# Kernel optimization log

Measured on AMD Instinct MI355X. Metric: run time of the kernel, lower is better.

The kernel has to match this reference:

```python
import jax, jax.numpy as jnp
import numpy as np
import math

B, S, H, N = 64, 512, 768, 16
C_COMP, C_REL = 5, 3
P = N * (N - 1)
LN_EPS = 1e-5

# ordered pair indices (i, j), i != j, row-major like the torch double loop
_PAIR_I, _PAIR_J = np.nonzero(~np.eye(N, dtype=bool))
_PAIR_I = jnp.asarray(_PAIR_I)
_PAIR_J = jnp.asarray(_PAIR_J)


def setup_inputs() -> dict:
    key = jax.random.key(0)
    ks = jax.random.split(key, 20)
    sc = 0.02
    p = lambda k, shape: (jax.random.normal(k, shape, jnp.float32) * sc)
    return {
        "last_hidden_state": jax.random.normal(ks[0], (B, S, H), jnp.float32),
        "span_starts": jax.random.randint(ks[1], (B, N), 0, 480).astype(jnp.int32),
        "span_lengths": jax.random.randint(ks[2], (B, N), 0, 31).astype(jnp.int32),
        "components": jax.random.randint(ks[3], (B, N), 0, C_COMP).astype(jnp.int32),
        "relations": jax.random.randint(ks[4], (B, P), 0, C_REL).astype(jnp.int32),
        # comp_classifier: Linear(H,512) -> Tanh -> Linear(512,C_COMP)
        "comp_w1": p(ks[5], (H, 512)), "comp_b1": jnp.zeros((512,), jnp.float32),
        "comp_w2": p(ks[6], (512, C_COMP)), "comp_b2": jnp.zeros((C_COMP,), jnp.float32),
        # Attention(H, H), no bias
        "wq": p(ks[7], (H, H)), "wk": p(ks[8], (H, H)), "wv": p(ks[9], (H, H)),
        # LayerNorm(H)
        "ln_g": jnp.ones((H,), jnp.float32), "ln_b": jnp.zeros((H,), jnp.float32),
        # rel_classifier: Linear(2H,512) -> Tanh -> Linear(512,C_REL)
        "rel_w1": p(ks[10], (2 * H, 512)), "rel_b1": jnp.zeros((512,), jnp.float32),
        "rel_w2": p(ks[11], (512, C_REL)), "rel_b2": jnp.zeros((C_REL,), jnp.float32),
    }


def _ce_mean(logits, gold):
    # logits [M, C], gold [M] -> scalar mean cross entropy
    logp = jax.nn.log_softmax(logits, axis=-1)
    return -jnp.mean(jnp.take_along_axis(logp, gold[:, None].astype(jnp.int32), axis=-1))


def reference(last_hidden_state, span_starts, span_lengths, components, relations,
              comp_w1, comp_b1, comp_w2, comp_b2,
              wq, wk, wv, ln_g, ln_b,
              rel_w1, rel_b1, rel_w2, rel_b2):
    # --- per-span mean pooling (inclusive end = start + length), masked+vectorized ---
    pos = jnp.arange(S)
    ends = span_starts + span_lengths
    mask = ((pos[None, None, :] >= span_starts[:, :, None]) &
            (pos[None, None, :] <= ends[:, :, None])).astype(jnp.float32)  # [B,N,S]
    lens = (span_lengths + 1).astype(jnp.float32)
    pooled = jnp.einsum('bns,bsh->bnh', mask, last_hidden_state) / lens[:, :, None]  # [B,N,H]
    # dropout(p=0.2) is identity in eval mode

    # --- component classifier ---
    comp_logits = jnp.tanh(pooled @ comp_w1 + comp_b1) @ comp_w2 + comp_b2  # [B,N,C_COMP]

    # --- small self-attention over spans ---
    q = pooled @ wq; k = pooled @ wk; v = pooled @ wv
    scores = jax.nn.softmax(jnp.einsum('bnd,bmd->bnm', q, k) / math.sqrt(H), axis=-1)
    attn = jnp.einsum('bnm,bmh->bnh', scores, v)

    # --- residual + layernorm ---
    x = pooled + attn
    mu = jnp.mean(x, axis=-1, keepdims=True)
    var = jnp.mean((x - mu) ** 2, axis=-1, keepdims=True)
    x = (x - mu) * jax.lax.rsqrt(var + LN_EPS) * ln_g + ln_b  # [B,N,H]

    # --- O(N^2) pairwise relation classification (ordered pairs i != j) ---
    pair_feat = jnp.concatenate([x[:, _PAIR_I, :], x[:, _PAIR_J, :]], axis=-1)  # [B,P,2H]
    rel_logits = jnp.tanh(pair_feat @ rel_w1 + rel_b1) @ rel_w2 + rel_b2  # [B,P,C_REL]

    loss_comp = _ce_mean(comp_logits.reshape(-1, C_COMP), components.reshape(-1))
    loss_rel = _ce_mean(rel_logits.reshape(-1, C_REL), relations.reshape(-1))
    return (comp_logits.reshape(-1, C_COMP), rel_logits.reshape(-1, C_REL), loss_comp, loss_rel)
```

## Files before the change

### kernel.cpp

```cpp
#include <hip/hip_runtime.h>

#define BB 64
#define SS 512
#define HH 768
#define NSPAN 16
#define PP 240
#define CCOMP 5
#define CREL 3

typedef unsigned short u16;
typedef __attribute__((ext_vector_type(8))) short bf16x8;
typedef __attribute__((ext_vector_type(4))) float f32x4;

__device__ __forceinline__ u16 f2bf(float f) {
    union { float f; unsigned int i; } v; v.f = f;
    unsigned int x = v.i;
    unsigned int lsb = (x >> 16) & 1u;
    x += 0x7fffu + lsb;
    return (u16)(x >> 16);
}

__device__ __forceinline__ float ftanh(float x) {
    float xc = fminf(fmaxf(x, -15.f), 15.f);
    float e = __expf(2.f * xc);
    return (e - 1.f) / (e + 1.f);
}

__global__ __launch_bounds__(256) void prep_kernel(
    const float* __restrict__ cw1, const float* __restrict__ wq,
    const float* __restrict__ wk, const float* __restrict__ wv,
    const float* __restrict__ rw1, u16* __restrict__ wcat_t, u16* __restrict__ relw_t) {
    int blk = blockIdx.x;
    const float* W; int ldw, nt; u16* outp;
    if (blk < 384)        {             W = cw1; ldw = 512; nt = 16; outp = wcat_t; }
    else if (blk < 960)   { blk -= 384; W = wq;  ldw = 768; nt = 24; outp = wcat_t + (size_t)512 * 768; }
    else if (blk < 1536)  { blk -= 960; W = wk;  ldw = 768; nt = 24; outp = wcat_t + (size_t)1280 * 768; }
    else if (blk < 2112)  { blk -= 1536; W = wv; ldw = 768; nt = 24; outp = wcat_t + (size_t)2048 * 768; }
    else if (blk < 2496)  { blk -= 2112; W = rw1; ldw = 512; nt = 16; outp = relw_t; }
    else                  { blk -= 2496; W = rw1 + (size_t)768 * 512; ldw = 512; nt = 16; outp = relw_t + (size_t)512 * 768; }
    int tk = blk / nt, tn = blk % nt;
    int k0 = tk * 32, n0 = tn * 32;
    __shared__ u16 Ls[32][36];
    int tid = threadIdx.x;
    int tx = tid & 31, ty = tid >> 5;
#pragma unroll
    for (int r = 0; r < 4; ++r) {
        int k = ty + r * 8;
        Ls[tx][k] = f2bf(W[(size_t)(k0 + k) * ldw + n0 + tx]);
    }
    __syncthreads();
#pragma unroll
    for (int r = 0; r < 4; ++r) {
        int n = ty + r * 8;
        outp[(size_t)(n0 + n) * 768 + k0 + tx] = Ls[n][tx];
    }
}

__global__ __launch_bounds__(256) void pool_kernel(
    const float* __restrict__ lhs, const int* __restrict__ starts,
    const int* __restrict__ lens, float* __restrict__ pooled, u16* __restrict__ pooled_bf) {
    int bn = blockIdx.x;
    int b = bn >> 4;
    int st = starts[bn];
    int ln = lens[bn];
    int tid = threadIdx.x;
    const float* base = lhs + ((size_t)b * SS + st) * HH;
    float a0 = 0.f, a1 = 0.f, a2 = 0.f;
    for (int s = 0; s <= ln; ++s) {
        const float* row = base + (size_t)s * HH;
        a0 += row[tid];
        a1 += row[tid + 256];
        a2 += row[tid + 512];
    }
    float inv = 1.0f / (float)(ln + 1);
    a0 *= inv; a1 *= inv; a2 *= inv;
    float* out = pooled + (size_t)bn * HH;
    u16* outb = pooled_bf + (size_t)bn * HH;
    out[tid] = a0;       out[tid + 256] = a1;       out[tid + 512] = a2;
    outb[tid] = f2bf(a0); outb[tid + 256] = f2bf(a1); outb[tid + 512] = f2bf(a2);
}

__global__ __launch_bounds__(256) void gemm_pw_kernel(
    const u16* __restrict__ pooled_bf, const u16* __restrict__ wcat_t,
    const float* __restrict__ comp_b1, float* __restrict__ y2) {
    __shared__ u16 As[64][72];
    __shared__ u16 Bs[64][72];
    int ccol0 = blockIdx.x * 64;
    int row0 = blockIdx.y * 64;
    int act = (ccol0 < 512);
    int tid = threadIdx.x;
    int lane = tid & 63, w = tid >> 6;
    int q = lane >> 4, l15 = lane & 15;
    int wm = (w & 1) * 32, wn = (w >> 1) * 32;
    int r = tid >> 2, c0 = (tid & 3) * 16;
    const u16* ga = pooled_bf + (size_t)(row0 + r) * 768 + c0;
    const u16* gb = wcat_t + (size_t)(ccol0 + r) * 768 + c0;
    f32x4 acc[2][2];
#pragma unroll
    for (int i = 0; i < 2; ++i)
#pragma unroll
        for (int j = 0; j < 2; ++j) acc[i][j] = (f32x4){0.f, 0.f, 0.f, 0.f};

    uint4 va0 = *(const uint4*)(ga);
    uint4 va1 = *(const uint4*)(ga + 8);
    uint4 vb0 = *(const uint4*)(gb);
    uint4 vb1 = *(const uint4*)(gb + 8);
    for (int k0 = 0; k0 < 768; k0 += 64) {
        __syncthreads();
        *(uint4*)(&As[r][c0]) = va0;
        *(uint4*)(&As[r][c0 + 8]) = va1;
        *(uint4*)(&Bs[r][c0]) = vb0;
        *(uint4*)(&Bs[r][c0 + 8]) = vb1;
        __syncthreads();
        if (k0 + 64 < 768) {
            va0 = *(const uint4*)(ga + k0 + 64);
            va1 = *(const uint4*)(ga + k0 + 72);
            vb0 = *(const uint4*)(gb + k0 + 64);
            vb1 = *(const uint4*)(gb + k0 + 72);
        }
#pragma unroll
        for (int ks = 0; ks < 2; ++ks) {
            bf16x8 a0 = *(const bf16x8*)(&As[wm + l15][ks * 32 + q * 8]);
            bf16x8 a1 = *(const bf16x8*)(&As[wm + 16 + l15][ks * 32 + q * 8]);
            bf16x8 b0 = *(const bf16x8*)(&Bs[wn + l15][ks * 32 + q * 8]);
            bf16x8 b1 = *(const bf16x8*)(&Bs[wn + 16 + l15][ks * 32 + q * 8]);
            acc[0][0] = __builtin_amdgcn_mfma_f32_16x16x32_bf16(a0, b0, acc[0][0], 0, 0, 0);
            acc[0][1] = __builtin_amdgcn_mfma_f32_16x16x32_bf16(a0, b1, acc[0][1], 0, 0, 0);
            acc[1][0] = __builtin_amdgcn_mfma_f32_16x16x32_bf16(a1, b0, acc[1][0], 0, 0, 0);
            acc[1][1] = __builtin_amdgcn_mfma_f32_16x16x32_bf16(a1, b1, acc[1][1], 0, 0, 0);
        }
    }
#pragma unroll
    for (int tm = 0; tm < 2; ++tm)
#pragma unroll
        for (int tn = 0; tn < 2; ++tn)
#pragma unroll
            for (int reg = 0; reg < 4; ++reg) {
                int rr = row0 + wm + tm * 16 + q * 4 + reg;
                int cc = ccol0 + wn + tn * 16 + l15;
                float v = acc[tm][tn][reg];
                if (act) v = ftanh(v + comp_b1[cc]);
                y2[(size_t)rr * 2816 + cc] = v;
            }
}

__global__ __launch_bounds__(256) void gemm_z_kernel(
    const u16* __restrict__ x_bf, const u16* __restrict__ relw_t, float* __restrict__ Z) {
    __shared__ u16 As[32][72];
    __shared__ u16 Bs[64][72];
    int ccol0 = blockIdx.x * 64;
    int row0 = blockIdx.y * 32;
    int tid = threadIdx.x;
    int lane = tid & 63, w = tid >> 6;
    int q = lane >> 4, l15 = lane & 15;
    int wm = (w & 1) * 16, wn = (w >> 1) * 32;
    int ra = tid >> 3, ca = (tid & 7) * 8;
    int rb = tid >> 2, cb = (tid & 3) * 16;
    const u16* ga = x_bf + (size_t)(row0 + ra) * 768 + ca;
    const u16* gb = relw_t + (size_t)(ccol0 + rb) * 768 + cb;
    f32x4 acc[2];
    acc[0] = (f32x4){0.f, 0.f, 0.f, 0.f};
    acc[1] = (f32x4){0.f, 0.f, 0.f, 0.f};

    uint4 va = *(const uint4*)(ga);
    uint4 vb0 = *(const uint4*)(gb);
    uint4 vb1 = *(const uint4*)(gb + 8);
    for (int k0 = 0; k0 < 768; k0 += 64) {
        __syncthreads();
        *(uint4*)(&As[ra][ca]) = va;
        *(uint4*)(&Bs[rb][cb]) = vb0;
        *(uint4*)(&Bs[rb][cb + 8]) = vb1;
        __syncthreads();
        if (k0 + 64 < 768) {
            va = *(const uint4*)(ga + k0 + 64);
            vb0 = *(const uint4*)(gb + k0 + 64);
            vb1 = *(const uint4*)(gb + k0 + 72);
        }
#pragma unroll
        for (int ks = 0; ks < 2; ++ks) {
            bf16x8 a0 = *(const bf16x8*)(&As[wm + l15][ks * 32 + q * 8]);
            bf16x8 b0 = *(const bf16x8*)(&Bs[wn + l15][ks * 32 + q * 8]);
            bf16x8 b1 = *(const bf16x8*)(&Bs[wn + 16 + l15][ks * 32 + q * 8]);
            acc[0] = __builtin_amdgcn_mfma_f32_16x16x32_bf16(a0, b0, acc[0], 0, 0, 0);
            acc[1] = __builtin_amdgcn_mfma_f32_16x16x32_bf16(a0, b1, acc[1], 0, 0, 0);
        }
    }
#pragma unroll
    for (int tn = 0; tn < 2; ++tn)
#pragma unroll
        for (int reg = 0; reg < 4; ++reg) {
            int rr = row0 + wm + q * 4 + reg;
            int cc = ccol0 + wn + tn * 16 + l15;
            Z[(size_t)rr * 1024 + cc] = acc[tn][reg];
        }
}

__global__ __launch_bounds__(256) void attn_ln_kernel(
    const float* __restrict__ y2, const float* __restrict__ pooled,
    const float* __restrict__ ln_g, const float* __restrict__ ln_b,
    u16* __restrict__ x_bf) {
    __shared__ float ks[16][772];
    __shared__ float Ssm[16][17];
    int b = blockIdx.x;
    int tid = threadIdx.x;
    int n = tid >> 4;
    int hl = tid & 15;

    for (int u = 0; u < 48; ++u) {
        int h = hl + (u << 4);
        ks[n][h] = y2[((size_t)(b * 16 + n)) * 2816 + 1280 + h];
    }
    __syncthreads();

    int m = tid & 15;
    const float* qrow = y2 + ((size_t)(b * 16 + n)) * 2816 + 512;
    float dot = 0.f;
    for (int h = 0; h < 768; h += 4) {
        float4 qv = *(const float4*)(qrow + h);
        float4 kv = *(const float4*)(&ks[m][h]);
        dot += qv.x * kv.x + qv.y * kv.y + qv.z * kv.z + qv.w * kv.w;
    }
    float sval = dot * 0.03608439182435161f;
    float mx = sval;
#pragma unroll
    for (int off = 8; off >= 1; off >>= 1) mx = fmaxf(mx, __shfl_xor(mx, off, 16));
    float pexp = __expf(sval - mx);
    float psum = pexp;
#pragma unroll
    for (int off = 8; off >= 1; off >>= 1) psum += __shfl_xor(psum, off, 16);
    Ssm[n][m] = pexp / psum;
    __syncthreads();

    for (int u = 0; u < 48; ++u) {
        int h = hl + (u << 4);
        ks[n][h] = y2[((size_t)(b * 16 + n)) * 2816 + 2048 + h];
    }
    __syncthreads();

    float sc[16];
#pragma unroll
    for (int mm = 0; mm < 16; ++mm) sc[mm] = Ssm[n][mm];
    int row = b * 16 + n;
    const float* prow = pooled + (size_t)row * HH;
    float xv[48];
    float ssum = 0.f, ssq = 0.f;
    for (int u = 0; u < 48; ++u) {
        int h = hl + (u << 4);
        float a = 0.f;
#pragma unroll
        for (int mm = 0; mm < 16; ++mm) a += sc[mm] * ks[mm][h];
        float v = prow[h] + a;
        xv[u] = v;
        ssum += v;
        ssq += v * v;
    }
#pragma unroll
    for (int off = 8; off >= 1; off >>= 1) {
        ssum += __shfl_xor(ssum, off, 16);
        ssq += __shfl_xor(ssq, off, 16);
    }
    float mu = ssum * (1.0f / 768.0f);
    float var = ssq * (1.0f / 768.0f) - mu * mu;
    float rs = rsqrtf(var + 1e-5f);
    u16* xrow_bf = x_bf + (size_t)row * HH;
    for (int u = 0; u < 48; ++u) {
        int h = hl + (u << 4);
        xrow_bf[h] = f2bf((xv[u] - mu) * rs * ln_g[h] + ln_b[h]);
    }
}

__global__ __launch_bounds__(256) void heads_kernel(
    const float* __restrict__ Z, const float* __restrict__ rb1,
    const float* __restrict__ rw2, const float* __restrict__ rb2,
    const int* __restrict__ rels,
    const float* __restrict__ y2, const float* __restrict__ cw2,
    const float* __restrict__ cb2, const int* __restrict__ comps,
    float* __restrict__ out, float* __restrict__ rel_p, float* __restrict__ comp_p) {
    __shared__ float red[4];
    int wave = threadIdx.x >> 6, lane = threadIdx.x & 63;
    if (blockIdx.x < 3840) {
        int row = blockIdx.x * 4 + wave;
        int b = row / PP;
        int p = row - b * PP;
        int i = p / 15;
        int jj = p - i * 15;
        int j = jj + (jj >= i ? 1 : 0);
        const float* z1 = Z + ((size_t)(b * 16 + i)) * 1024;
        const float* z2 = Z + ((size_t)(b * 16 + j)) * 1024 + 512;
        float a0 = 0.f, a1 = 0.f, a2 = 0.f;
#pragma unroll
        for (int t = 0; t < 8; ++t) {
            int c = lane + (t << 6);
            float h = ftanh(z1[c] + z2[c] + rb1[c]);
            a0 += h * rw2[c * 3 + 0];
            a1 += h * rw2[c * 3 + 1];
            a2 += h * rw2[c * 3 + 2];
        }
#pragma unroll
        for (int off = 32; off >= 1; off >>= 1) {
            a0 += __shfl_down(a0, off);
            a1 += __shfl_down(a1, off);
            a2 += __shfl_down(a2, off);
        }
        if (lane == 0) {
            float l0 = a0 + rb2[0];
            float l1 = a1 + rb2[1];
            float l2 = a2 + rb2[2];
            float mx = fmaxf(l0, fmaxf(l1, l2));
            float se = __expf(l0 - mx) + __expf(l1 - mx) + __expf(l2 - mx);
            float lse = __logf(se) + mx;
            int g = rels[row];
            float lg = (g == 0) ? l0 : ((g == 1) ? l1 : l2);
            red[wave] = lse - lg;
            float* o = out + 5120 + (size_t)row * 3;
            o[0] = l0; o[1] = l1; o[2] = l2;
        }
        __syncthreads();
        if (threadIdx.x == 0) rel_p[blockIdx.x] = red[0] + red[1] + red[2] + red[3];
    } else {
        int row = (blockIdx.x - 3840) * 4 + wave;
        const float* hrow = y2 + (size_t)row * 2816;
        float acc[CCOMP] = {0.f, 0.f, 0.f, 0.f, 0.f};
#pragma unroll
        for (int t = 0; t < 8; ++t) {
            int c = lane + (t << 6);
            float h = hrow[c];
#pragma unroll
            for (int cc = 0; cc < CCOMP; ++cc) acc[cc] += h * cw2[c * CCOMP + cc];
        }
#pragma unroll
        for (int cc = 0; cc < CCOMP; ++cc)
#pragma unroll
            for (int off = 32; off >= 1; off >>= 1) acc[cc] += __shfl_down(acc[cc], off);
        if (lane == 0) {
            float l[CCOMP];
            float mx = -1e30f;
#pragma unroll
            for (int cc = 0; cc < CCOMP; ++cc) { l[cc] = acc[cc] + cb2[cc]; mx = fmaxf(mx, l[cc]); }
            float se = 0.f;
#pragma unroll
            for (int cc = 0; cc < CCOMP; ++cc) se += __expf(l[cc] - mx);
            float lse = __logf(se) + mx;
            red[wave] = lse - l[comps[row]];
#pragma unroll
            for (int cc = 0; cc < CCOMP; ++cc) out[row * CCOMP + cc] = l[cc];
        }
        __syncthreads();
        if (threadIdx.x == 0) comp_p[blockIdx.x - 3840] = red[0] + red[1] + red[2] + red[3];
    }
}

__global__ __launch_bounds__(256) void finalize_kernel(
    const float* __restrict__ comp_p, const float* __restrict__ rel_p,
    float* __restrict__ out) {
    __shared__ float rc[4], rr[4];
    int tid = threadIdx.x;
    int wave = tid >> 6, lane = tid & 63;
    float sc = comp_p[tid];
    float sr = 0.f;
#pragma unroll
    for (int k = 0; k < 15; ++k) sr += rel_p[tid + k * 256];
#pragma unroll
    for (int off = 32; off >= 1; off >>= 1) {
        sc += __shfl_down(sc, off);
        sr += __shfl_down(sr, off);
    }
    if (lane == 0) { rc[wave] = sc; rr[wave] = sr; }
    __syncthreads();
    if (tid == 0) {
        out[51200] = (rc[0] + rc[1] + rc[2] + rc[3]) * (1.0f / 1024.0f);
        out[51201] = (rr[0] + rr[1] + rr[2] + rr[3]) * (1.0f / 15360.0f);
    }
}

extern "C" void kernel_launch(void* const* d_in, const int* in_sizes, int n_in,
                              void* d_out, int out_size, void* d_ws, size_t ws_size,
                              hipStream_t stream) {
    const float* lhs     = (const float*)d_in[0];
    const int* starts    = (const int*)d_in[1];
    const int* lens      = (const int*)d_in[2];
    const int* comps     = (const int*)d_in[3];
    const int* rels      = (const int*)d_in[4];
    const float* comp_w1 = (const float*)d_in[5];
    const float* comp_b1 = (const float*)d_in[6];
    const float* comp_w2 = (const float*)d_in[7];
    const float* comp_b2 = (const float*)d_in[8];
    const float* wq      = (const float*)d_in[9];
    const float* wk      = (const float*)d_in[10];
    const float* wv      = (const float*)d_in[11];
    const float* ln_g    = (const float*)d_in[12];
    const float* ln_b    = (const float*)d_in[13];
    const float* rel_w1  = (const float*)d_in[14];
    const float* rel_b1  = (const float*)d_in[15];
    const float* rel_w2  = (const float*)d_in[16];
    const float* rel_b2  = (const float*)d_in[17];
    float* out = (float*)d_out;
    float* ws = (float*)d_ws;

    float* pooled = ws;
    float* y2     = pooled + 786432;
    float* Z      = y2 + 2883584;
    float* comp_p = Z + 1048576;
    float* rel_p  = comp_p + 256;
    u16* pooled_bf = (u16*)(rel_p + 3840);
    u16* x_bf      = pooled_bf + 786432;
    u16* wcat_t    = x_bf + 786432;
    u16* relw_t    = wcat_t + 2162688;

    prep_kernel<<<2880, 256, 0, stream>>>(comp_w1, wq, wk, wv, rel_w1, wcat_t, relw_t);
    pool_kernel<<<1024, 256, 0, stream>>>(lhs, starts, lens, pooled, pooled_bf);
    gemm_pw_kernel<<<dim3(44, 16), 256, 0, stream>>>(pooled_bf, wcat_t, comp_b1, y2);
    attn_ln_kernel<<<64, 256, 0, stream>>>(y2, pooled, ln_g, ln_b, x_bf);
    gemm_z_kernel<<<dim3(16, 32), 256, 0, stream>>>(x_bf, relw_t, Z);
    heads_kernel<<<4096, 256, 0, stream>>>(Z, rel_b1, rel_w2, rel_b2, rels,
                                           y2, comp_w2, comp_b2, comps,
                                           out, rel_p, comp_p);
    finalize_kernel<<<1, 256, 0, stream>>>(comp_p, rel_p, out);
}
```

Measured before the change: 243.2 us.

## Merge small kernels to cut launch count and fold finalize into last block

Combines the weight-prep and pooling kernels into one launch. Moves the component-head computation into the attention/LayerNorm launch as extra blocks. Replaces the separate finalize kernel with a last-block-done atomic counter inside the relation head kernel. This cuts seven launches to five, removing launch gaps and tail idle time. It adds an atomic counter and threadfence, and correctness depends on the counter being reset in the first kernel.

```diff
diff --git a/kernel.cpp b/kernel.cpp
--- a/kernel.cpp
+++ b/kernel.cpp
@@ -3,7 +3,6 @@
 #define BB 64
 #define SS 512
 #define HH 768
-#define NSPAN 16
 #define PP 240
 #define CCOMP 5
 #define CREL 3
@@ -19,65 +18,65 @@
     x += 0x7fffu + lsb;
     return (u16)(x >> 16);
 }
-
 __device__ __forceinline__ float ftanh(float x) {
     float xc = fminf(fmaxf(x, -15.f), 15.f);
     float e = __expf(2.f * xc);
     return (e - 1.f) / (e + 1.f);
 }
 
-__global__ __launch_bounds__(256) void prep_kernel(
+__global__ __launch_bounds__(256) void prep_pool_kernel(
     const float* __restrict__ cw1, const float* __restrict__ wq,
     const float* __restrict__ wk, const float* __restrict__ wv,
-    const float* __restrict__ rw1, u16* __restrict__ wcat_t, u16* __restrict__ relw_t) {
-    int blk = blockIdx.x;
-    const float* W; int ldw, nt; u16* outp;
-    if (blk < 384)        {             W = cw1; ldw = 512; nt = 16; outp = wcat_t; }
-    else if (blk < 960)   { blk -= 384; W = wq;  ldw = 768; nt = 24; outp = wcat_t + (size_t)512 * 768; }
-    else if (blk < 1536)  { blk -= 960; W = wk;  ldw = 768; nt = 24; outp = wcat_t + (size_t)1280 * 768; }
-    else if (blk < 2112)  { blk -= 1536; W = wv; ldw = 768; nt = 24; outp = wcat_t + (size_t)2048 * 768; }
-    else if (blk < 2496)  { blk -= 2112; W = rw1; ldw = 512; nt = 16; outp = relw_t; }
-    else                  { blk -= 2496; W = rw1 + (size_t)768 * 512; ldw = 512; nt = 16; outp = relw_t + (size_t)512 * 768; }
-    int tk = blk / nt, tn = blk % nt;
-    int k0 = tk * 32, n0 = tn * 32;
+    const float* __restrict__ rw1, u16* __restrict__ wcat_t, u16* __restrict__ relw_t,
+    const float* __restrict__ lhs, const int* __restrict__ starts,
+    const int* __restrict__ lens, float* __restrict__ pooled, u16* __restrict__ pooled_bf,
+    unsigned int* __restrict__ counter) {
     __shared__ u16 Ls[32][36];
     int tid = threadIdx.x;
-    int tx = tid & 31, ty = tid >> 5;
-#pragma unroll
-    for (int r = 0; r < 4; ++r) {
-        int k = ty + r * 8;
-        Ls[tx][k] = f2bf(W[(size_t)(k0 + k) * ldw + n0 + tx]);
-    }
-    __syncthreads();
-#pragma unroll
-    for (int r = 0; r < 4; ++r) {
-        int n = ty + r * 8;
-        outp[(size_t)(n0 + n) * 768 + k0 + tx] = Ls[n][tx];
-    }
-}
-
-__global__ __launch_bounds__(256) void pool_kernel(
-    const float* __restrict__ lhs, const int* __restrict__ starts,
-    const int* __restrict__ lens, float* __restrict__ pooled, u16* __restrict__ pooled_bf) {
-    int bn = blockIdx.x;
-    int b = bn >> 4;
-    int st = starts[bn];
-    int ln = lens[bn];
-    int tid = threadIdx.x;
-    const float* base = lhs + ((size_t)b * SS + st) * HH;
-    float a0 = 0.f, a1 = 0.f, a2 = 0.f;
-    for (int s = 0; s <= ln; ++s) {
-        const float* row = base + (size_t)s * HH;
-        a0 += row[tid];
-        a1 += row[tid + 256];
-        a2 += row[tid + 512];
-    }
-    float inv = 1.0f / (float)(ln + 1);
-    a0 *= inv; a1 *= inv; a2 *= inv;
-    float* out = pooled + (size_t)bn * HH;
-    u16* outb = pooled_bf + (size_t)bn * HH;
-    out[tid] = a0;       out[tid + 256] = a1;       out[tid + 512] = a2;
-    outb[tid] = f2bf(a0); outb[tid + 256] = f2bf(a1); outb[tid + 512] = f2bf(a2);
+    if (blockIdx.x == 0 && tid == 0) *counter = 0u;
+    if (blockIdx.x < 2880) {
+        int blk = blockIdx.x;
+        const float* W; int ldw, nt; u16* outp;
+        if (blk < 384)        {             W = cw1; ldw = 512; nt = 16; outp = wcat_t; }
+        else if (blk < 960)   { blk -= 384; W = wq;  ldw = 768; nt = 24; outp = wcat_t + (size_t)512 * 768; }
+        else if (blk < 1536)  { blk -= 960; W = wk;  ldw = 768; nt = 24; outp = wcat_t + (size_t)1280 * 768; }
+        else if (blk < 2112)  { blk -= 1536; W = wv; ldw = 768; nt = 24; outp = wcat_t + (size_t)2048 * 768; }
+        else if (blk < 2496)  { blk -= 2112; W = rw1; ldw = 512; nt = 16; outp = relw_t; }
+        else                  { blk -= 2496; W = rw1 + (size_t)768 * 512; ldw = 512; nt = 16; outp = relw_t + (size_t)512 * 768; }
+        int tk = blk / nt, tn = blk % nt;
+        int k0 = tk * 32, n0 = tn * 32;
+        int tx = tid & 31, ty = tid >> 5;
+#pragma unroll
+        for (int r = 0; r < 4; ++r) {
+            int k = ty + r * 8;
+            Ls[tx][k] = f2bf(W[(size_t)(k0 + k) * ldw + n0 + tx]);
+        }
+        __syncthreads();
+#pragma unroll
+        for (int r = 0; r < 4; ++r) {
+            int n = ty + r * 8;
+            outp[(size_t)(n0 + n) * 768 + k0 + tx] = Ls[n][tx];
+        }
+    } else {
+        int bn = blockIdx.x - 2880;
+        int b = bn >> 4;
+        int st = starts[bn];
+        int ln = lens[bn];
+        const float* base = lhs + ((size_t)b * SS + st) * HH;
+        float a0 = 0.f, a1 = 0.f, a2 = 0.f;
+        for (int s = 0; s <= ln; ++s) {
+            const float* row = base + (size_t)s * HH;
+            a0 += row[tid];
+            a1 += row[tid + 256];
+            a2 += row[tid + 512];
+        }
+        float inv = 1.0f / (float)(ln + 1);
+        a0 *= inv; a1 *= inv; a2 *= inv;
+        float* o = pooled + (size_t)bn * HH;
+        u16* ob = pooled_bf + (size_t)bn * HH;
+        o[tid] = a0;        o[tid + 256] = a1;        o[tid + 512] = a2;
+        ob[tid] = f2bf(a0); ob[tid + 256] = f2bf(a1); ob[tid + 512] = f2bf(a2);
+    }
 }
 
 __global__ __launch_bounds__(256) void gemm_pw_kernel(
@@ -142,6 +141,113 @@
                 if (act) v = ftanh(v + comp_b1[cc]);
                 y2[(size_t)rr * 2816 + cc] = v;
             }
+}
+
+__global__ __launch_bounds__(256) void attn_comp_kernel(
+    const float* __restrict__ y2, const float* __restrict__ pooled,
+    const float* __restrict__ ln_g, const float* __restrict__ ln_b,
+    u16* __restrict__ x_bf,
+    const float* __restrict__ cw2, const float* __restrict__ cb2,
+    const int* __restrict__ comps, float* __restrict__ out, float* __restrict__ comp_p) {
+    __shared__ __align__(16) char smem[50560];
+    int tid = threadIdx.x;
+    if (blockIdx.x < 64) {
+        float (*ks)[772] = (float(*)[772])smem;
+        float (*Ssm)[17] = (float(*)[17])(smem + 49408);
+        int b = blockIdx.x;
+        int n = tid >> 4;
+        int hl = tid & 15;
+        for (int u = 0; u < 48; ++u) {
+            int h = hl + (u << 4);
+            ks[n][h] = y2[((size_t)(b * 16 + n)) * 2816 + 1280 + h];
+        }
+        __syncthreads();
+        int m = tid & 15;
+        const float* qrow = y2 + ((size_t)(b * 16 + n)) * 2816 + 512;
+        float dot = 0.f;
+        for (int h = 0; h < 768; h += 4) {
+            float4 qv = *(const float4*)(qrow + h);
+            float4 kv = *(const float4*)(&ks[m][h]);
+            dot += qv.x * kv.x + qv.y * kv.y + qv.z * kv.z + qv.w * kv.w;
+        }
+        float sval = dot * 0.03608439182435161f;
+        float mx = sval;
+#pragma unroll
+        for (int off = 8; off >= 1; off >>= 1) mx = fmaxf(mx, __shfl_xor(mx, off, 16));
+        float pexp = __expf(sval - mx);
+        float psum = pexp;
+#pragma unroll
+        for (int off = 8; off >= 1; off >>= 1) psum += __shfl_xor(psum, off, 16);
+        Ssm[n][m] = pexp / psum;
+        __syncthreads();
+        for (int u = 0; u < 48; ++u) {
+            int h = hl + (u << 4);
+            ks[n][h] = y2[((size_t)(b * 16 + n)) * 2816 + 2048 + h];
+        }
+        __syncthreads();
+        float sc[16];
+#pragma unroll
+        for (int mm = 0; mm < 16; ++mm) sc[mm] = Ssm[n][mm];
+        int row = b * 16 + n;
+        const float* prow = pooled + (size_t)row * HH;
+        float xv[48];
+        float ssum = 0.f, ssq = 0.f;
+        for (int u = 0; u < 48; ++u) {
+            int h = hl + (u << 4);
+            float a = 0.f;
+#pragma unroll
+            for (int mm = 0; mm < 16; ++mm) a += sc[mm] * ks[mm][h];
+            float v = prow[h] + a;
+            xv[u] = v;
+            ssum += v;
+            ssq += v * v;
+        }
+#pragma unroll
+        for (int off = 8; off >= 1; off >>= 1) {
+            ssum += __shfl_xor(ssum, off, 16);
+            ssq += __shfl_xor(ssq, off, 16);
+        }
+        float mu = ssum * (1.0f / 768.0f);
+        float var = ssq * (1.0f / 768.0f) - mu * mu;
+        float rs = rsqrtf(var + 1e-5f);
+        u16* xrow_bf = x_bf + (size_t)row * HH;
+        for (int u = 0; u < 48; ++u) {
+            int h = hl + (u << 4);
+            xrow_bf[h] = f2bf((xv[u] - mu) * rs * ln_g[h] + ln_b[h]);
+        }
+    } else {
+        float* red = (float*)smem;
+        int wave = tid >> 6, lane = tid & 63;
+        int row = (blockIdx.x - 64) * 4 + wave;
+        const float* hrow = y2 + (size_t)row * 2816;
+        float acc[CCOMP] = {0.f, 0.f, 0.f, 0.f, 0.f};
+#pragma unroll
+        for (int t = 0; t < 8; ++t) {
+            int c = lane + (t << 6);
+            float h = hrow[c];
+#pragma unroll
+            for (int cc = 0; cc < CCOMP; ++cc) acc[cc] += h * cw2[c * CCOMP + cc];
+        }
+#pragma unroll
+        for (int cc = 0; cc < CCOMP; ++cc)
+#pragma unroll
+            for (int off = 32; off >= 1; off >>= 1) acc[cc] += __shfl_down(acc[cc], off);
+        if (lane == 0) {
+            float l[CCOMP];
+            float mx = -1e30f;
+#pragma unroll
+            for (int cc = 0; cc < CCOMP; ++cc) { l[cc] = acc[cc] + cb2[cc]; mx = fmaxf(mx, l[cc]); }
+            float se = 0.f;
+#pragma unroll
+            for (int cc = 0; cc < CCOMP; ++cc) se += __expf(l[cc] - mx);
+            float lse = __logf(se) + mx;
+            red[wave] = lse - l[comps[row]];
+#pragma unroll
+            for (int cc = 0; cc < CCOMP; ++cc) out[row * CCOMP + cc] = l[cc];
+        }
+        __syncthreads();
+        if (tid == 0) comp_p[blockIdx.x - 64] = red[0] + red[1] + red[2] + red[3];
+    }
 }
 
 __global__ __launch_bounds__(256) void gemm_z_kernel(
@@ -195,181 +301,78 @@
         }
 }
 
-__global__ __launch_bounds__(256) void attn_ln_kernel(
-    const float* __restrict__ y2, const float* __restrict__ pooled,
-    const float* __restrict__ ln_g, const float* __restrict__ ln_b,
-    u16* __restrict__ x_bf) {
-    __shared__ float ks[16][772];
-    __shared__ float Ssm[16][17];
-    int b = blockIdx.x;
-    int tid = threadIdx.x;
-    int n = tid >> 4;
-    int hl = tid & 15;
-
-    for (int u = 0; u < 48; ++u) {
-        int h = hl + (u << 4);
-        ks[n][h] = y2[((size_t)(b * 16 + n)) * 2816 + 1280 + h];
-    }
-    __syncthreads();
-
-    int m = tid & 15;
-    const float* qrow = y2 + ((size_t)(b * 16 + n)) * 2816 + 512;
-    float dot = 0.f;
-    for (int h = 0; h < 768; h += 4) {
-        float4 qv = *(const float4*)(qrow + h);
-        float4 kv = *(const float4*)(&ks[m][h]);
-        dot += qv.x * kv.x + qv.y * kv.y + qv.z * kv.z + qv.w * kv.w;
-    }
-    float sval = dot * 0.03608439182435161f;
-    float mx = sval;
-#pragma unroll
-    for (int off = 8; off >= 1; off >>= 1) mx = fmaxf(mx, __shfl_xor(mx, off, 16));
-    float pexp = __expf(sval - mx);
-    float psum = pexp;
-#pragma unroll
-    for (int off = 8; off >= 1; off >>= 1) psum += __shfl_xor(psum, off, 16);
-    Ssm[n][m] = pexp / psum;
-    __syncthreads();
-
-    for (int u = 0; u < 48; ++u) {
-        int h = hl + (u << 4);
-        ks[n][h] = y2[((size_t)(b * 16 + n)) * 2816 + 2048 + h];
-    }
-    __syncthreads();
-
-    float sc[16];
-#pragma unroll
-    for (int mm = 0; mm < 16; ++mm) sc[mm] = Ssm[n][mm];
-    int row = b * 16 + n;
-    const float* prow = pooled + (size_t)row * HH;
-    float xv[48];
-    float ssum = 0.f, ssq = 0.f;
-    for (int u = 0; u < 48; ++u) {
-        int h = hl + (u << 4);
-        float a = 0.f;
-#pragma unroll
-        for (int mm = 0; mm < 16; ++mm) a += sc[mm] * ks[mm][h];
-        float v = prow[h] + a;
-        xv[u] = v;
-        ssum += v;
-        ssq += v * v;
-    }
-#pragma unroll
-    for (int off = 8; off >= 1; off >>= 1) {
-        ssum += __shfl_xor(ssum, off, 16);
-        ssq += __shfl_xor(ssq, off, 16);
-    }
-    float mu = ssum * (1.0f / 768.0f);
-    float var = ssq * (1.0f / 768.0f) - mu * mu;
-    float rs = rsqrtf(var + 1e-5f);
-    u16* xrow_bf = x_bf + (size_t)row * HH;
-    for (int u = 0; u < 48; ++u) {
-        int h = hl + (u << 4);
-        xrow_bf[h] = f2bf((xv[u] - mu) * rs * ln_g[h] + ln_b[h]);
-    }
-}
-
-__global__ __launch_bounds__(256) void heads_kernel(
-    const float* __restrict__ Z, const float* __restrict__ rb1,
-    const float* __restrict__ rw2, const float* __restrict__ rb2,
-    const int* __restrict__ rels,
-    const float* __restrict__ y2, const float* __restrict__ cw2,
-    const float* __restrict__ cb2, const int* __restrict__ comps,
-    float* __restrict__ out, float* __restrict__ rel_p, float* __restrict__ comp_p) {
+__global__ __launch_bounds__(256) void rel_final_kernel(
+    const float* __restrict__ Z, const float* __restrict__ b1,
+    const float* __restrict__ w2, const float* __restrict__ b2,
+    const int* __restrict__ gold, float* __restrict__ out,
+    float* __restrict__ rel_p, const float* __restrict__ comp_p,
+    unsigned int* __restrict__ counter) {
     __shared__ float red[4];
-    int wave = threadIdx.x >> 6, lane = threadIdx.x & 63;
-    if (blockIdx.x < 3840) {
-        int row = blockIdx.x * 4 + wave;
-        int b = row / PP;
-        int p = row - b * PP;
-        int i = p / 15;
-        int jj = p - i * 15;
-        int j = jj + (jj >= i ? 1 : 0);
-        const float* z1 = Z + ((size_t)(b * 16 + i)) * 1024;
-        const float* z2 = Z + ((size_t)(b * 16 + j)) * 1024 + 512;
-        float a0 = 0.f, a1 = 0.f, a2 = 0.f;
-#pragma unroll
-        for (int t = 0; t < 8; ++t) {
-            int c = lane + (t << 6);
-            float h = ftanh(z1[c] + z2[c] + rb1[c]);
-            a0 += h * rw2[c * 3 + 0];
-            a1 += h * rw2[c * 3 + 1];
-            a2 += h * rw2[c * 3 + 2];
-        }
-#pragma unroll
-        for (int off = 32; off >= 1; off >>= 1) {
-            a0 += __shfl_down(a0, off);
-            a1 += __shfl_down(a1, off);
-            a2 += __shfl_down(a2, off);
-        }
-        if (lane == 0) {
-            float l0 = a0 + rb2[0];
-            float l1 = a1 + rb2[1];
-            float l2 = a2 + rb2[2];
-            float mx = fmaxf(l0, fmaxf(l1, l2));
-            float se = __expf(l0 - mx) + __expf(l1 - mx) + __expf(l2 - mx);
-            float lse = __logf(se) + mx;
-            int g = rels[row];
-            float lg = (g == 0) ? l0 : ((g == 1) ? l1 : l2);
-            red[wave] = lse - lg;
-            float* o = out + 5120 + (size_t)row * 3;
-            o[0] = l0; o[1] = l1; o[2] = l2;
-        }
-        __syncthreads();
-        if (threadIdx.x == 0) rel_p[blockIdx.x] = red[0] + red[1] + red[2] + red[3];
-    } else {
-        int row = (blockIdx.x - 3840) * 4 + wave;
-        const float* hrow = y2 + (size_t)row * 2816;
-        float acc[CCOMP] = {0.f, 0.f, 0.f, 0.f, 0.f};
-#pragma unroll
-        for (int t = 0; t < 8; ++t) {
-            int c = lane + (t << 6);
-            float h = hrow[c];
-#pragma unroll
-            for (int cc = 0; cc < CCOMP; ++cc) acc[cc] += h * cw2[c * CCOMP + cc];
-        }
-#pragma unroll
-        for (int cc = 0; cc < CCOMP; ++cc)
-#pragma unroll
-            for (int off = 32; off >= 1; off >>= 1) acc[cc] += __shfl_down(acc[cc], off);
-        if (lane == 0) {
-            float l[CCOMP];
-            float mx = -1e30f;
-#pragma unroll
-            for (int cc = 0; cc < CCOMP; ++cc) { l[cc] = acc[cc] + cb2[cc]; mx = fmaxf(mx, l[cc]); }
-            float se = 0.f;
-#pragma unroll
-            for (int cc = 0; cc < CCOMP; ++cc) se += __expf(l[cc] - mx);
-            float lse = __logf(se) + mx;
-            red[wave] = lse - l[comps[row]];
-#pragma unroll
-            for (int cc = 0; cc < CCOMP; ++cc) out[row * CCOMP + cc] = l[cc];
-        }
-        __syncthreads();
-        if (threadIdx.x == 0) comp_p[blockIdx.x - 3840] = red[0] + red[1] + red[2] + red[3];
-    }
-}
-
-__global__ __launch_bounds__(256) void finalize_kernel(
-    const float* __restrict__ comp_p, const float* __restrict__ rel_p,
-    float* __restrict__ out) {
-    __shared__ float rc[4], rr[4];
+    __shared__ int isLast;
     int tid = threadIdx.x;
     int wave = tid >> 6, lane = tid & 63;
-    float sc = comp_p[tid];
-    float sr = 0.f;
-#pragma unroll
-    for (int k = 0; k < 15; ++k) sr += rel_p[tid + k * 256];
+    int row = blockIdx.x * 4 + wave;
+    int b = row / PP;
+    int p = row - b * PP;
+    int i = p / 15;
+    int jj = p - i * 15;
+    int j = jj + (jj >= i ? 1 : 0);
+    const float* z1 = Z + ((size_t)(b * 16 + i)) * 1024;
+    const float* z2 = Z + ((size_t)(b * 16 + j)) * 1024 + 512;
+    float a0 = 0.f, a1 = 0.f, a2 = 0.f;
+#pragma unroll
+    for (int t = 0; t < 8; ++t) {
+        int c = lane + (t << 6);
+        float h = ftanh(z1[c] + z2[c] + b1[c]);
+        a0 += h * w2[c * 3 + 0];
+        a1 += h * w2[c * 3 + 1];
+        a2 += h * w2[c * 3 + 2];
+    }
 #pragma unroll
     for (int off = 32; off >= 1; off >>= 1) {
-        sc += __shfl_down(sc, off);
-        sr += __shfl_down(sr, off);
-    }
-    if (lane == 0) { rc[wave] = sc; rr[wave] = sr; }
+        a0 += __shfl_down(a0, off);
+        a1 += __shfl_down(a1, off);
+        a2 += __shfl_down(a2, off);
+    }
+    if (lane == 0) {
+        float l0 = a0 + b2[0];
+        float l1 = a1 + b2[1];
+        float l2 = a2 + b2[2];
+        float mx = fmaxf(l0, fmaxf(l1, l2));
+        float se = __expf(l0 - mx) + __expf(l1 - mx) + __expf(l2 - mx);
+        float lse = __logf(se) + mx;
+        int g = gold[row];
+        float lg = (g == 0) ? l0 : ((g == 1) ? l1 : l2);
+        red[wave] = lse - lg;
+        float* o = out + 5120 + (size_t)row * 3;
+        o[0] = l0; o[1] = l1; o[2] = l2;
+    }
     __syncthreads();
     if (tid == 0) {
-        out[51200] = (rc[0] + rc[1] + rc[2] + rc[3]) * (1.0f / 1024.0f);
-        out[51201] = (rr[0] + rr[1] + rr[2] + rr[3]) * (1.0f / 15360.0f);
+        rel_p[blockIdx.x] = red[0] + red[1] + red[2] + red[3];
+        __threadfence();
+        unsigned int prev = atomicAdd(counter, 1u);
+        isLast = (prev == 3839u);
+    }
+    __syncthreads();
+    if (isLast) {
+        __threadfence();
+        __shared__ float rc[4], rr[4];
+        float sc = comp_p[tid];
+        float sr = 0.f;
+#pragma unroll
+        for (int k = 0; k < 15; ++k) sr += rel_p[tid + k * 256];
+#pragma unroll
+        for (int off = 32; off >= 1; off >>= 1) {
+            sc += __shfl_down(sc, off);
+            sr += __shfl_down(sr, off);
+        }
+        if (lane == 0) { rc[wave] = sc; rr[wave] = sr; }
+        __syncthreads();
+        if (tid == 0) {
+            out[51200] = (rc[0] + rc[1] + rc[2] + rc[3]) * (1.0f / 1024.0f);
+            out[51201] = (rr[0] + rr[1] + rr[2] + rr[3]) * (1.0f / 15360.0f);
+        }
     }
 }
 
@@ -402,18 +405,18 @@
     float* Z      = y2 + 2883584;
     float* comp_p = Z + 1048576;
     float* rel_p  = comp_p + 256;
-    u16* pooled_bf = (u16*)(rel_p + 3840);
+    unsigned int* counter = (unsigned int*)(rel_p + 3840);
+    u16* pooled_bf = (u16*)(counter + 4);
     u16* x_bf      = pooled_bf + 786432;
     u16* wcat_t    = x_bf + 786432;
     u16* relw_t    = wcat_t + 2162688;
 
-    prep_kernel<<<2880, 256, 0, stream>>>(comp_w1, wq, wk, wv, rel_w1, wcat_t, relw_t);
-    pool_kernel<<<1024, 256, 0, stream>>>(lhs, starts, lens, pooled, pooled_bf);
+    prep_pool_kernel<<<3904, 256, 0, stream>>>(comp_w1, wq, wk, wv, rel_w1, wcat_t, relw_t,
+                                               lhs, starts, lens, pooled, pooled_bf, counter);
     gemm_pw_kernel<<<dim3(44, 16), 256, 0, stream>>>(pooled_bf, wcat_t, comp_b1, y2);
-    attn_ln_kernel<<<64, 256, 0, stream>>>(y2, pooled, ln_g, ln_b, x_bf);
+    attn_comp_kernel<<<320, 256, 0, stream>>>(y2, pooled, ln_g, ln_b, x_bf,
+                                              comp_w2, comp_b2, comps, out, comp_p);
     gemm_z_kernel<<<dim3(16, 32), 256, 0, stream>>>(x_bf, relw_t, Z);
-    heads_kernel<<<4096, 256, 0, stream>>>(Z, rel_b1, rel_w2, rel_b2, rels,
-                                           y2, comp_w2, comp_b2, comps,
-                                           out, rel_p, comp_p);
-    finalize_kernel<<<1, 256, 0, stream>>>(comp_p, rel_p, out);
-}
+    rel_final_kernel<<<3840, 256, 0, stream>>>(Z, rel_b1, rel_w2, rel_b2, rels,
+                                               out, rel_p, comp_p, counter);
+}
```

Measured after the change: 328.2 us. 1.35x slower.
